# Optimization experiments

Measured on AMD Instinct MI355X. Metric: run time of the kernel, lower is better.

## Reference

```python
import jax, jax.numpy as jnp
import numpy as np

N, C, H, W = 8, 256, 64, 64  # C == dim_inner

def conv1x1(x, w, b):
    # x: [N,C,H,W], w: [O,C], b: [O]  (1x1 conv == per-pixel matmul)
    return jnp.einsum('oc,nchw->nohw', w, x) + b[None, :, None, None]

def setup_inputs() -> dict:
    key = jax.random.key(0)
    ks = jax.random.split(key, 10)
    s = 1.0 / np.sqrt(C)
    return {
        'x':       jax.random.normal(ks[0], (N, C, H, W), dtype=jnp.float32),
        'w_theta': jax.random.uniform(ks[1], (C, C), jnp.float32, -s, s),
        'b_theta': jax.random.uniform(ks[2], (C,),   jnp.float32, -s, s),
        'w_phi':   jax.random.uniform(ks[3], (C, C), jnp.float32, -s, s),
        'b_phi':   jax.random.uniform(ks[4], (C,),   jnp.float32, -s, s),
        'w_g':     jax.random.uniform(ks[5], (C, C), jnp.float32, -s, s),
        'b_g':     jax.random.uniform(ks[6], (C,),   jnp.float32, -s, s),
        'w_out':   jax.random.uniform(ks[7], (C, C), jnp.float32, -s, s),
        'b_out':   jax.random.uniform(ks[8], (C,),   jnp.float32, -s, s),
        'gamma':   jnp.ones((C,), jnp.float32),
        'beta':    jnp.zeros((C,), jnp.float32),
        'w_gate':  jnp.asarray(0.5, jnp.float32),
    }

def reference(x, w_theta, b_theta, w_phi, b_phi, w_g, b_g, w_out, b_out, gamma, beta, w_gate):
    norm_eps = 1e-5
    x_identity = x
    theta = conv1x1(x, w_theta, b_theta).reshape(N, C, H * W)
    phi   = conv1x1(x, w_phi,   b_phi  ).reshape(N, C, H * W)
    g     = conv1x1(x, w_g,     b_g    ).reshape(N, C, H * W)
    # [N, HW, HW] attention scores
    theta_phi = jnp.einsum('nch,ncp->nhp', theta, phi) * (C ** -0.5)
    theta_phi = jax.nn.softmax(theta_phi, axis=2)
    theta_phi_g = jnp.einsum('nhg,ncg->nch', theta_phi, g).reshape(N, C, H, W)
    p = conv1x1(theta_phi_g, w_out, b_out)
    # BatchNorm2d in training mode: batch stats over (N,H,W), biased var
    mean = p.mean(axis=(0, 2, 3))
    var = p.var(axis=(0, 2, 3))
    p = (p - mean[None, :, None, None]) * jax.lax.rsqrt(var + norm_eps)[None, :, None, None]
    p = p * gamma[None, :, None, None] + beta[None, :, None, None]
    z = (1.0 - w_gate) * x_identity + w_gate * p
    return z
```

## Files before the change

kernel.cpp:

```cpp
#include <hip/hip_runtime.h>

#define N_ 8
#define C_ 256
#define HW_ 4096
#define KVBLK 64

typedef __bf16 bf16x8 __attribute__((ext_vector_type(8)));
typedef float f32x4 __attribute__((ext_vector_type(4)));
typedef float f32x16 __attribute__((ext_vector_type(16)));
typedef unsigned short u16x8 __attribute__((ext_vector_type(8)));
typedef unsigned int uint2v __attribute__((ext_vector_type(2)));

#define MFMA(a, b, c)   __builtin_amdgcn_mfma_f32_16x16x32_bf16(a, b, c, 0, 0, 0)
#define MFMA32(a, b, c) __builtin_amdgcn_mfma_f32_32x32x16_bf16(a, b, c, 0, 0, 0)

static __device__ __forceinline__ unsigned short f2bf(float f) {
    union { float f; unsigned int u; } v; v.f = f;
    unsigned int u = v.u;
    return (unsigned short)((u + 0x7FFFu + ((u >> 16) & 1u)) >> 16);
}

static __device__ __forceinline__ bf16x8 pack_bf8(float4 a, float4 b) {
    u16x8 t;
    t[0] = f2bf(a.x); t[1] = f2bf(a.y); t[2] = f2bf(a.z); t[3] = f2bf(a.w);
    t[4] = f2bf(b.x); t[5] = f2bf(b.y); t[6] = f2bf(b.z); t[7] = f2bf(b.w);
    return __builtin_bit_cast(bf16x8, t);
}

static __device__ __forceinline__ unsigned cvt_pk_bf16(float lo, float hi) {
    unsigned r;
    asm("v_cvt_pk_bf16_f32 %0, %1, %2" : "=v"(r) : "v"(lo), "v"(hi));
    return r;
}

static __device__ __forceinline__ void plswap(unsigned& a, unsigned& b) {
#if __has_builtin(__builtin_amdgcn_permlane32_swap)
    uint2v r = __builtin_amdgcn_permlane32_swap(a, b, false, false);
    a = r[0]; b = r[1];
#else
    asm volatile("v_permlane32_swap_b32 %0, %1" : "+v"(a), "+v"(b));
#endif
}

#define GLOAD_LDS16(src, dst)                                                   \
    __builtin_amdgcn_global_load_lds(                                           \
        (const __attribute__((address_space(1))) unsigned int*)(const void*)(src), \
        (__attribute__((address_space(3))) unsigned int*)(void*)(dst), 16, 0, 0)

__global__ __launch_bounds__(256) void qkv_kernel(
    const float* __restrict__ x,
    const float* __restrict__ w_theta, const float* __restrict__ b_theta,
    const float* __restrict__ w_phi,   const float* __restrict__ b_phi,
    const float* __restrict__ w_g,     const float* __restrict__ b_g,
    unsigned short* __restrict__ thetaT, unsigned short* __restrict__ phiT,
    unsigned short* __restrict__ gC)
{
    __shared__ unsigned short xT[64 * 264];
    __shared__ unsigned short tile[64 * 72];
    const int tid = threadIdx.x;
    const int hw0 = blockIdx.x * 64;
    const int n   = blockIdx.y;
    const float* xb = x + (size_t)n * C_ * HW_;
    for (int i = 0; i < 16; ++i) {
        int e   = tid + i * 256;
        int c   = e >> 4;
        int hw4 = (e & 15) << 2;
        float4 v = *reinterpret_cast<const float4*>(xb + (size_t)c * HW_ + hw0 + hw4);
        xT[(hw4 + 0) * 264 + c] = f2bf(v.x);
        xT[(hw4 + 1) * 264 + c] = f2bf(v.y);
        xT[(hw4 + 2) * 264 + c] = f2bf(v.z);
        xT[(hw4 + 3) * 264 + c] = f2bf(v.w);
    }
    __syncthreads();

    const int w = tid >> 6, lane = tid & 63;
    const int g16 = lane >> 4, l16 = lane & 15;

    const float* Wp[3] = { w_theta, w_phi, w_g };
    const float* Bp[3] = { b_theta, b_phi, b_g };

    for (int ot = 0; ot < 4; ++ot) {
        const int oB    = ot * 64;
        const int wrow  = oB + w * 16 + l16;
        const int orow0 = oB + w * 16 + g16 * 4;
        #pragma unroll
        for (int wt = 0; wt < 3; ++wt) {
            const float* W = Wp[wt];
            bf16x8 aw[8];
            #pragma unroll
            for (int kk = 0; kk < 8; ++kk) {
                const float* wp = W + (size_t)wrow * C_ + kk * 32 + g16 * 8;
                float4 f0 = *reinterpret_cast<const float4*>(wp);
                float4 f1 = *reinterpret_cast<const float4*>(wp + 4);
                aw[kk] = pack_bf8(f0, f1);
            }
            f32x4 acc[4];
            #pragma unroll
            for (int cb = 0; cb < 4; ++cb) {
                acc[cb][0] = 0.f; acc[cb][1] = 0.f; acc[cb][2] = 0.f; acc[cb][3] = 0.f;
            }
            #pragma unroll
            for (int kk = 0; kk < 8; ++kk) {
                #pragma unroll
                for (int cb = 0; cb < 4; ++cb) {
                    bf16x8 b = *reinterpret_cast<const bf16x8*>(
                        &xT[(cb * 16 + l16) * 264 + kk * 32 + g16 * 8]);
                    acc[cb] = MFMA(aw[kk], b, acc[cb]);
                }
            }
            const float* bp = Bp[wt];
            float bj0 = bp[orow0], bj1 = bp[orow0 + 1], bj2 = bp[orow0 + 2], bj3 = bp[orow0 + 3];
            if (wt == 2) { bj0 = 0.f; bj1 = 0.f; bj2 = 0.f; bj3 = 0.f; }
            if (wt < 2) {
                const float sc = (wt == 0) ? 0.0625f : 1.0f;
                __syncthreads();
                #pragma unroll
                for (int cb = 0; cb < 4; ++cb) {
                    ushort4 pk;
                    pk.x = f2bf((acc[cb][0] + bj0) * sc);
                    pk.y = f2bf((acc[cb][1] + bj1) * sc);
                    pk.z = f2bf((acc[cb][2] + bj2) * sc);
                    pk.w = f2bf((acc[cb][3] + bj3) * sc);
                    *reinterpret_cast<ushort4*>(&tile[(cb * 16 + l16) * 72 + w * 16 + g16 * 4]) = pk;
                }
                __syncthreads();
                unsigned short* dst = (wt == 0) ? thetaT : phiT;
                #pragma unroll
                for (int i = 0; i < 2; ++i) {
                    int e = tid + i * 256;
                    int row = e >> 3, seg = (e & 7) << 3;
                    *reinterpret_cast<uint4*>(
                        &dst[((size_t)n * HW_ + hw0 + row) * C_ + oB + seg]) =
                        *reinterpret_cast<const uint4*>(&tile[row * 72 + seg]);
                }
            } else {
                #pragma unroll
                for (int cb = 0; cb < 4; ++cb) {
                    int hw = hw0 + cb * 16 + l16;
                    gC[((size_t)n * C_ + orow0 + 0) * HW_ + hw] = f2bf(acc[cb][0]);
                    gC[((size_t)n * C_ + orow0 + 1) * HW_ + hw] = f2bf(acc[cb][1]);
                    gC[((size_t)n * C_ + orow0 + 2) * HW_ + hw] = f2bf(acc[cb][2]);
                    gC[((size_t)n * C_ + orow0 + 3) * HW_ + hw] = f2bf(acc[cb][3]);
                }
            }
        }
    }
}

__global__ __launch_bounds__(256, 1) void attn_kernel(
    const unsigned short* __restrict__ thetaT,
    const unsigned short* __restrict__ phiT,
    const unsigned short* __restrict__ gC,
    unsigned short* __restrict__ tpgT)
{
    __shared__ __align__(16) unsigned short Kbuf[2][64 * 256];
    __shared__ __align__(16) unsigned short Vbuf[2][256 * 64];

    const int tid  = threadIdx.x;
    const int bid  = blockIdx.x;
    const int n    = bid & 7;
    const int qt   = bid >> 3;
    const int w    = tid >> 6, lane = tid & 63;
    const int l31  = lane & 31;
    const int hi   = lane >> 5;
    const int hi8  = hi << 3;

    const unsigned short* Kb = phiT + (size_t)n * HW_ * C_;
    const unsigned short* Vb = gC   + (size_t)n * C_ * HW_;

    bf16x8 qf[16];
    {
        const unsigned short* qp = thetaT + ((size_t)n * HW_ + qt * 128 + w * 32 + l31) * C_;
        #pragma unroll
        for (int kk = 0; kk < 16; ++kk)
            qf[kk] = *reinterpret_cast<const bf16x8*>(qp + kk * 16 + hi8);
    }

    f32x16 oacc[8];
    #pragma unroll
    for (int ncb = 0; ncb < 8; ++ncb)
        #pragma unroll
        for (int r = 0; r < 16; ++r) oacc[ncb][r] = 0.f;
    float m = -1e30f, l = 0.f;

    const int vrow_lane = lane >> 3;
    const int vslot_x   = ((lane & 7) ^ vrow_lane) << 3;

#define STAGE(buf, kv0)                                                          \
    do {                                                                         \
        _Pragma("unroll")                                                        \
        for (int i = 0; i < 8; ++i) {                                            \
            const int rl = w * 16 + i * 2 + hi;                                  \
            const unsigned short* src =                                          \
                Kb + (size_t)((kv0) + rl) * C_ + ((l31 ^ (rl & 31)) << 3);       \
            GLOAD_LDS16(src, &Kbuf[buf][(w * 16 + i * 2) * 256]);                \
        }                                                                        \
        _Pragma("unroll")                                                        \
        for (int i = 0; i < 8; ++i) {                                            \
            const int cr = w * 64 + i * 8 + vrow_lane;                           \
            const unsigned short* src = Vb + (size_t)cr * HW_ + (kv0) + vslot_x; \
            GLOAD_LDS16(src, &Vbuf[buf][(w * 64 + i * 8) * 64]);                 \
        }                                                                        \
    } while (0)

    STAGE(0, 0);
    __syncthreads();

    for (int t = 0; t < 64; ++t) {
        const int cur = t & 1;
        if (t < 63) STAGE(cur ^ 1, (t + 1) * KVBLK);

        f32x16 st[2];
        #pragma unroll
        for (int T = 0; T < 2; ++T) {
            f32x16 sA, sB;
            #pragma unroll
            for (int r = 0; r < 16; ++r) { sA[r] = 0.f; sB[r] = 0.f; }
            const unsigned short* Krow = &Kbuf[cur][(T * 32 + l31) * 256];
            const int swz = l31 << 3;
            #pragma unroll
            for (int kk = 0; kk < 8; ++kk) {
                bf16x8 af = *reinterpret_cast<const bf16x8*>(Krow + (((kk * 16) + hi8) ^ swz));
                sA = MFMA32(af, qf[kk], sA);
            }
            #pragma unroll
            for (int kk = 8; kk < 16; ++kk) {
                bf16x8 af = *reinterpret_cast<const bf16x8*>(Krow + (((kk * 16) + hi8) ^ swz));
                sB = MFMA32(af, qf[kk], sB);
            }
            st[T] = sA + sB;
        }

        float own = st[0][0];
        #pragma unroll
        for (int r = 1; r < 16; ++r) own = fmaxf(own, st[0][r]);
        #pragma unroll
        for (int r = 0; r < 16; ++r) own = fmaxf(own, st[1][r]);
        float pmax = fmaxf(own, __shfl_xor(own, 32));
        if (__any(pmax > m + 8.f)) {
            float mn = fmaxf(m, pmax);
            float f  = __expf(m - mn);
            m = mn; l *= f;
            #pragma unroll
            for (int r = 0; r < 16; ++r) {
                int qr = (r & 3) + 8 * (r >> 2) + (hi8 >> 1);
                float fr = __shfl(f, qr);
                #pragma unroll
                for (int ncb = 0; ncb < 8; ++ncb) oacc[ncb][r] *= fr;
            }
        }
        float lsum = 0.f;
        #pragma unroll
        for (int T = 0; T < 2; ++T)
            #pragma unroll
            for (int r = 0; r < 16; ++r) {
                float e = __expf(st[T][r] - m);
                lsum += e;
                st[T][r] = e;
            }
        l += lsum;

        #pragma unroll
        for (int T = 0; T < 2; ++T) {
            #pragma unroll
            for (int g = 0; g < 2; ++g) {
                unsigned w0 = cvt_pk_bf16(st[T][g * 8 + 0], st[T][g * 8 + 1]);
                unsigned w1 = cvt_pk_bf16(st[T][g * 8 + 2], st[T][g * 8 + 3]);
                unsigned w2 = cvt_pk_bf16(st[T][g * 8 + 4], st[T][g * 8 + 5]);
                unsigned w3 = cvt_pk_bf16(st[T][g * 8 + 6], st[T][g * 8 + 7]);
                plswap(w0, w2);
                plswap(w1, w3);
                uint4 pw; pw.x = w0; pw.y = w1; pw.z = w2; pw.w = w3;
                bf16x8 pf = __builtin_bit_cast(bf16x8, pw);
                const int kk2 = T * 2 + g;
                #pragma unroll
                for (int ncb = 0; ncb < 8; ++ncb) {
                    const int vr = ncb * 32 + l31;
                    bf16x8 vf = *reinterpret_cast<const bf16x8*>(
                        &Vbuf[cur][vr * 64 + (((kk2 * 16) + hi8) ^ ((vr & 7) << 3))]);
                    oacc[ncb] = MFMA32(pf, vf, oacc[ncb]);
                }
            }
        }
        __syncthreads();
    }
#undef STAGE

    float l_tot = l + __shfl_xor(l, 32);
    float inv = 1.0f / l_tot;
    unsigned short* op = tpgT + ((size_t)n * HW_ + qt * 128 + w * 32) * C_;
    #pragma unroll
    for (int r = 0; r < 16; ++r) {
        int qr = (r & 3) + 8 * (r >> 2) + (hi8 >> 1);
        float Lir = __shfl(inv, qr);
        #pragma unroll
        for (int ncb = 0; ncb < 8; ++ncb)
            op[(size_t)qr * C_ + ncb * 32 + l31] = f2bf(oacc[ncb][r] * Lir);
    }
}

__global__ __launch_bounds__(256) void outconv_kernel(
    const unsigned short* __restrict__ tpgT,
    const float* __restrict__ w_out, const float* __restrict__ b_out,
    float* __restrict__ p, float* __restrict__ bnsum, float* __restrict__ bnsumsq)
{
    __shared__ unsigned short Bl[64 * 264];
    const int tid = threadIdx.x;
    const int hw0 = blockIdx.x * 64;
    const int n   = blockIdx.y;
    const unsigned short* Tb = tpgT + (size_t)n * HW_ * C_;
    for (int i = 0; i < 8; ++i) {
        int e = tid + i * 256;
        int r = e >> 5, c8 = (e & 31) << 3;
        *reinterpret_cast<uint4*>(&Bl[r * 264 + c8]) =
            *reinterpret_cast<const uint4*>(Tb + ((size_t)hw0 + r) * C_ + c8);
    }
    __syncthreads();
    const int w = tid >> 6, lane = tid & 63, g16 = lane >> 4, l16 = lane & 15;

    for (int ot = 0; ot < 4; ++ot) {
        const int oB   = ot * 64;
        const int wrow = oB + w * 16 + l16;
        bf16x8 aw[8];
        #pragma unroll
        for (int kk = 0; kk < 8; ++kk) {
            const float* wp = w_out + (size_t)wrow * C_ + kk * 32 + g16 * 8;
            float4 f0 = *reinterpret_cast<const float4*>(wp);
            float4 f1 = *reinterpret_cast<const float4*>(wp + 4);
            aw[kk] = pack_bf8(f0, f1);
        }
        f32x4 acc[4];
        #pragma unroll
        for (int cb = 0; cb < 4; ++cb) { acc[cb][0]=0.f; acc[cb][1]=0.f; acc[cb][2]=0.f; acc[cb][3]=0.f; }
        #pragma unroll
        for (int kk = 0; kk < 8; ++kk) {
            #pragma unroll
            for (int cb = 0; cb < 4; ++cb) {
                bf16x8 b = *reinterpret_cast<const bf16x8*>(
                    &Bl[(cb * 16 + l16) * 264 + kk * 32 + g16 * 8]);
                acc[cb] = MFMA(aw[kk], b, acc[cb]);
            }
        }
        const int orow0 = oB + w * 16 + g16 * 4;
        float bj[4] = { b_out[orow0], b_out[orow0 + 1], b_out[orow0 + 2], b_out[orow0 + 3] };
        float s1[4] = {0.f,0.f,0.f,0.f}, s2[4] = {0.f,0.f,0.f,0.f};
        #pragma unroll
        for (int cb = 0; cb < 4; ++cb) {
            #pragma unroll
            for (int j = 0; j < 4; ++j) {
                float pv = acc[cb][j] + bj[j];
                p[((size_t)n * C_ + orow0 + j) * HW_ + hw0 + cb * 16 + l16] = pv;
                s1[j] += pv;
                s2[j] += pv * pv;
            }
        }
        #pragma unroll
        for (int j = 0; j < 4; ++j) {
            float a1 = s1[j], a2 = s2[j];
            a1 += __shfl_xor(a1, 1); a2 += __shfl_xor(a2, 1);
            a1 += __shfl_xor(a1, 2); a2 += __shfl_xor(a2, 2);
            a1 += __shfl_xor(a1, 4); a2 += __shfl_xor(a2, 4);
            a1 += __shfl_xor(a1, 8); a2 += __shfl_xor(a2, 8);
            if (l16 == 0) {
                atomicAdd(&bnsum[orow0 + j], a1);
                atomicAdd(&bnsumsq[orow0 + j], a2);
            }
        }
    }
}

__global__ void bnfin_kernel(const float* __restrict__ bnsum,
                             const float* __restrict__ bnsumsq,
                             const float* __restrict__ gamma,
                             const float* __restrict__ beta,
                             float* __restrict__ bnscale, float* __restrict__ bnshift)
{
    int c = threadIdx.x;
    const float cnt = (float)(N_ * HW_);
    float mean = bnsum[c] / cnt;
    float var  = bnsumsq[c] / cnt - mean * mean;
    float inv  = rsqrtf(var + 1e-5f);
    float sc   = gamma[c] * inv;
    bnscale[c] = sc;
    bnshift[c] = beta[c] - mean * sc;
}

__global__ __launch_bounds__(256) void final_kernel(
    const float* __restrict__ x, const float* __restrict__ p,
    const float* __restrict__ bnscale, const float* __restrict__ bnshift,
    const float* __restrict__ wgate, float* __restrict__ out)
{
    const float wg = *wgate;
    const float og = 1.0f - wg;
    const int total = N_ * C_ * HW_ / 4;
    for (int e = blockIdx.x * 256 + threadIdx.x; e < total; e += gridDim.x * 256) {
        int c = (e >> 10) & 255;
        float sc = bnscale[c], sh = bnshift[c];
        float4 xv = reinterpret_cast<const float4*>(x)[e];
        float4 pv = reinterpret_cast<const float4*>(p)[e];
        float4 z;
        z.x = og * xv.x + wg * (pv.x * sc + sh);
        z.y = og * xv.y + wg * (pv.y * sc + sh);
        z.z = og * xv.z + wg * (pv.z * sc + sh);
        z.w = og * xv.w + wg * (pv.w * sc + sh);
        reinterpret_cast<float4*>(out)[e] = z;
    }
}

extern "C" void kernel_launch(void* const* d_in, const int* in_sizes, int n_in,
                              void* d_out, int out_size, void* d_ws, size_t ws_size,
                              hipStream_t stream)
{
    (void)in_sizes; (void)n_in; (void)out_size; (void)ws_size;
    const float* x       = (const float*)d_in[0];
    const float* w_theta = (const float*)d_in[1];
    const float* b_theta = (const float*)d_in[2];
    const float* w_phi   = (const float*)d_in[3];
    const float* b_phi   = (const float*)d_in[4];
    const float* w_g     = (const float*)d_in[5];
    const float* b_g     = (const float*)d_in[6];
    const float* w_out   = (const float*)d_in[7];
    const float* b_out   = (const float*)d_in[8];
    const float* gamma   = (const float*)d_in[9];
    const float* beta    = (const float*)d_in[10];
    const float* wgate   = (const float*)d_in[11];
    float* out = (float*)d_out;

    char* ws = (char*)d_ws;
    unsigned short* thetaT = (unsigned short*)(ws + 0);
    unsigned short* phiT   = (unsigned short*)(ws + 16777216);
    unsigned short* gC     = (unsigned short*)(ws + 33554432);
    unsigned short* tpgT   = (unsigned short*)(ws + 50331648);
    float* p       = (float*)(ws + 0);
    float* bnsum   = (float*)(ws + 67108864);
    float* bnsumsq = (float*)(ws + 67108864 + 1024);
    float* bnscale = (float*)(ws + 67108864 + 2048);
    float* bnshift = (float*)(ws + 67108864 + 3072);

    hipMemsetAsync(bnsum, 0, 2048, stream);

    qkv_kernel<<<dim3(64, 8), 256, 0, stream>>>(
        x, w_theta, b_theta, w_phi, b_phi, w_g, b_g, thetaT, phiT, gC);
    attn_kernel<<<dim3(256), 256, 0, stream>>>(thetaT, phiT, gC, tpgT);
    outconv_kernel<<<dim3(64, 8), 256, 0, stream>>>(tpgT, w_out, b_out, p, bnsum, bnsumsq);
    bnfin_kernel<<<1, 256, 0, stream>>>(bnsum, bnsumsq, gamma, beta, bnscale, bnshift);
    final_kernel<<<dim3(2048), 256, 0, stream>>>(x, p, bnscale, bnshift, wgate, out);
}
```

Measured before the change: 480.7 us.

## Split attention over two KV halves with a merge kernel

Adds a split-KV flash attention path. Each block handles a 128-query tile over half of the keys, using 32-wide KV stages and two blocks per CU, which doubles the grid to 512 blocks to improve occupancy and load balance on 256 CUs. Partial outputs in bf16 and the (m, l) statistics are written to workspace, and a separate merge kernel combines them by log-sum-exp rescaling. This costs extra global traffic, one more launch and an additional bf16 rounding of the partials. The original kernel stays as a fallback when the workspace is too small.

Result: slower. 492.5 us (+2.4%).

```diff
diff --git a/kernel.cpp b/kernel.cpp
--- a/kernel.cpp
+++ b/kernel.cpp
@@ -3,7 +3,6 @@
 #define N_ 8
 #define C_ 256
 #define HW_ 4096
-#define KVBLK 64
 
 typedef __bf16 bf16x8 __attribute__((ext_vector_type(8)));
 typedef float f32x4 __attribute__((ext_vector_type(4)));
@@ -18,6 +17,10 @@
     union { float f; unsigned int u; } v; v.f = f;
     unsigned int u = v.u;
     return (unsigned short)((u + 0x7FFFu + ((u >> 16) & 1u)) >> 16);
+}
+
+static __device__ __forceinline__ float bfu2f(unsigned s) {
+    union { unsigned u; float f; } v; v.u = s << 16; return v.f;
 }
 
 static __device__ __forceinline__ bf16x8 pack_bf8(float4 a, float4 b) {
@@ -147,7 +150,189 @@
     }
 }
 
-__global__ __launch_bounds__(256, 1) void attn_kernel(
+__global__ __launch_bounds__(256, 2) void attn_split_kernel(
+    const unsigned short* __restrict__ thetaT,
+    const unsigned short* __restrict__ phiT,
+    const unsigned short* __restrict__ gC,
+    unsigned short* __restrict__ Opart,
+    float2* __restrict__ ml)
+{
+    __shared__ __align__(16) unsigned short Kbuf[2][32 * 256];
+    __shared__ __align__(16) unsigned short Vbuf[2][256 * 32];
+
+    const int tid  = threadIdx.x;
+    const int bid  = blockIdx.x;
+    const int n    = bid & 7;
+    const int enc  = bid >> 3;
+    const int qt   = enc >> 1;
+    const int kvh  = enc & 1;
+    const int w    = tid >> 6, lane = tid & 63;
+    const int l31  = lane & 31;
+    const int hi   = lane >> 5;
+    const int hi8  = hi << 3;
+    const int kvbase = kvh * 2048;
+
+    const unsigned short* Kb = phiT + (size_t)n * HW_ * C_;
+    const unsigned short* Vb = gC   + (size_t)n * C_ * HW_;
+
+    bf16x8 qf[16];
+    {
+        const unsigned short* qp = thetaT + ((size_t)n * HW_ + qt * 128 + w * 32 + l31) * C_;
+        #pragma unroll
+        for (int kk = 0; kk < 16; ++kk)
+            qf[kk] = *reinterpret_cast<const bf16x8*>(qp + kk * 16 + hi8);
+    }
+
+    f32x16 oacc[8];
+    #pragma unroll
+    for (int ncb = 0; ncb < 8; ++ncb)
+        #pragma unroll
+        for (int r = 0; r < 16; ++r) oacc[ncb][r] = 0.f;
+    float m = -1e30f, l = 0.f;
+
+    const int vrow_lane = lane >> 2;
+    const int vslot     = lane & 3;
+
+#define STAGE(buf, kv0)                                                          \
+    do {                                                                         \
+        _Pragma("unroll")                                                        \
+        for (int i = 0; i < 4; ++i) {                                            \
+            const int rl = w * 8 + i * 2 + hi;                                   \
+            const unsigned short* src =                                          \
+                Kb + (size_t)((kv0) + rl) * C_ + ((l31 ^ rl) << 3);              \
+            GLOAD_LDS16(src, &Kbuf[buf][(w * 8 + i * 2) * 256]);                 \
+        }                                                                        \
+        _Pragma("unroll")                                                        \
+        for (int i = 0; i < 4; ++i) {                                            \
+            const int cr = w * 64 + i * 16 + vrow_lane;                          \
+            const unsigned short* src =                                          \
+                Vb + (size_t)cr * HW_ + (kv0) + ((vslot ^ ((cr >> 1) & 3)) << 3);\
+            GLOAD_LDS16(src, &Vbuf[buf][(w * 64 + i * 16) * 32]);                \
+        }                                                                        \
+    } while (0)
+
+    STAGE(0, kvbase);
+    __syncthreads();
+
+    for (int t = 0; t < 64; ++t) {
+        const int cur = t & 1;
+        if (t < 63) STAGE(cur ^ 1, kvbase + (t + 1) * 32);
+
+        f32x16 sA, sB;
+        #pragma unroll
+        for (int r = 0; r < 16; ++r) { sA[r] = 0.f; sB[r] = 0.f; }
+        const unsigned short* Krow = &Kbuf[cur][l31 * 256];
+        const int swz = l31 << 3;
+        #pragma unroll
+        for (int kk = 0; kk < 8; ++kk) {
+            bf16x8 af = *reinterpret_cast<const bf16x8*>(Krow + (((kk * 16) + hi8) ^ swz));
+            sA = MFMA32(af, qf[kk], sA);
+        }
+        #pragma unroll
+        for (int kk = 8; kk < 16; ++kk) {
+            bf16x8 af = *reinterpret_cast<const bf16x8*>(Krow + (((kk * 16) + hi8) ^ swz));
+            sB = MFMA32(af, qf[kk], sB);
+        }
+        f32x16 s = sA + sB;
+
+        float own = s[0];
+        #pragma unroll
+        for (int r = 1; r < 16; ++r) own = fmaxf(own, s[r]);
+        float pmax = fmaxf(own, __shfl_xor(own, 32));
+        if (__any(pmax > m + 8.f)) {
+            float mn = fmaxf(m, pmax);
+            float f  = __expf(m - mn);
+            m = mn; l *= f;
+            #pragma unroll
+            for (int r = 0; r < 16; ++r) {
+                int qr = (r & 3) + 8 * (r >> 2) + (hi8 >> 1);
+                float fr = __shfl(f, qr);
+                #pragma unroll
+                for (int ncb = 0; ncb < 8; ++ncb) oacc[ncb][r] *= fr;
+            }
+        }
+        float lsum = 0.f;
+        #pragma unroll
+        for (int r = 0; r < 16; ++r) {
+            float ex = __expf(s[r] - m);
+            lsum += ex;
+            s[r] = ex;
+        }
+        l += lsum;
+
+        #pragma unroll
+        for (int g = 0; g < 2; ++g) {
+            unsigned w0 = cvt_pk_bf16(s[g * 8 + 0], s[g * 8 + 1]);
+            unsigned w1 = cvt_pk_bf16(s[g * 8 + 2], s[g * 8 + 3]);
+            unsigned w2 = cvt_pk_bf16(s[g * 8 + 4], s[g * 8 + 5]);
+            unsigned w3 = cvt_pk_bf16(s[g * 8 + 6], s[g * 8 + 7]);
+            plswap(w0, w2);
+            plswap(w1, w3);
+            uint4 pw; pw.x = w0; pw.y = w1; pw.z = w2; pw.w = w3;
+            bf16x8 pf = __builtin_bit_cast(bf16x8, pw);
+            #pragma unroll
+            for (int ncb = 0; ncb < 8; ++ncb) {
+                const int vr = ncb * 32 + l31;
+                bf16x8 vf = *reinterpret_cast<const bf16x8*>(
+                    &Vbuf[cur][vr * 32 + (((g * 16) + hi8) ^ (((vr >> 1) & 3) << 3))]);
+                oacc[ncb] = MFMA32(pf, vf, oacc[ncb]);
+            }
+        }
+        __syncthreads();
+    }
+#undef STAGE
+
+    float l_tot = l + __shfl_xor(l, 32);
+    #pragma unroll
+    for (int r = 0; r < 16; ++r) {
+        int qr = (r & 3) + 8 * (r >> 2) + (hi8 >> 1);
+        #pragma unroll
+        for (int ncb = 0; ncb < 8; ++ncb)
+            Opart[((size_t)bid * 128 + w * 32 + qr) * 256 + ncb * 32 + l31] =
+                f2bf(oacc[ncb][r]);
+    }
+    if (lane < 32)
+        ml[(size_t)bid * 128 + w * 32 + l31] = make_float2(m, l_tot);
+}
+
+__global__ __launch_bounds__(256) void merge_kernel(
+    const unsigned short* __restrict__ Opart,
+    const float2* __restrict__ ml,
+    unsigned short* __restrict__ tpgT)
+{
+    const int b   = blockIdx.x;
+    const int n   = b & 7, qt = b >> 3;
+    const int tid = threadIdx.x;
+    const int r8  = tid >> 5;
+    const int c8  = (tid & 31) * 8;
+    const int b0  = ((qt * 2 + 0) << 3) | n;
+    const int b1  = ((qt * 2 + 1) << 3) | n;
+    for (int it = 0; it < 16; ++it) {
+        const int q = it * 8 + r8;
+        float2 a1 = ml[(size_t)b0 * 128 + q];
+        float2 a2 = ml[(size_t)b1 * 128 + q];
+        float M  = fmaxf(a1.x, a2.x);
+        float f1 = __expf(a1.x - M);
+        float f2 = __expf(a2.x - M);
+        float Li = 1.0f / (a1.y * f1 + a2.y * f2);
+        uint4 o1 = *reinterpret_cast<const uint4*>(&Opart[((size_t)b0 * 128 + q) * 256 + c8]);
+        uint4 o2 = *reinterpret_cast<const uint4*>(&Opart[((size_t)b1 * 128 + q) * 256 + c8]);
+        uint4 ov;
+        const unsigned* p1 = reinterpret_cast<const unsigned*>(&o1);
+        const unsigned* p2 = reinterpret_cast<const unsigned*>(&o2);
+        unsigned* po = reinterpret_cast<unsigned*>(&ov);
+        #pragma unroll
+        for (int k = 0; k < 4; ++k) {
+            float vlo = (bfu2f(p1[k] & 0xffffu) * f1 + bfu2f(p2[k] & 0xffffu) * f2) * Li;
+            float vhi = (bfu2f(p1[k] >> 16)     * f1 + bfu2f(p2[k] >> 16)     * f2) * Li;
+            po[k] = cvt_pk_bf16(vlo, vhi);
+        }
+        *reinterpret_cast<uint4*>(
+            &tpgT[((size_t)n * HW_ + qt * 128 + q) * 256 + c8]) = ov;
+    }
+}
+
+__global__ __launch_bounds__(256, 1) void attn_full_kernel(
     const unsigned short* __restrict__ thetaT,
     const unsigned short* __restrict__ phiT,
     const unsigned short* __restrict__ gC,
@@ -208,7 +393,7 @@
 
     for (int t = 0; t < 64; ++t) {
         const int cur = t & 1;
-        if (t < 63) STAGE(cur ^ 1, (t + 1) * KVBLK);
+        if (t < 63) STAGE(cur ^ 1, (t + 1) * 64);
 
         f32x16 st[2];
         #pragma unroll
@@ -254,9 +439,9 @@
         for (int T = 0; T < 2; ++T)
             #pragma unroll
             for (int r = 0; r < 16; ++r) {
-                float e = __expf(st[T][r] - m);
-                lsum += e;
-                st[T][r] = e;
+                float ex = __expf(st[T][r] - m);
+                lsum += ex;
+                st[T][r] = ex;
             }
         l += lsum;
 
@@ -411,7 +596,7 @@
                               void* d_out, int out_size, void* d_ws, size_t ws_size,
                               hipStream_t stream)
 {
-    (void)in_sizes; (void)n_in; (void)out_size; (void)ws_size;
+    (void)in_sizes; (void)n_in; (void)out_size;
     const float* x       = (const float*)d_in[0];
     const float* w_theta = (const float*)d_in[1];
     const float* b_theta = (const float*)d_in[2];
@@ -430,19 +615,41 @@
     unsigned short* thetaT = (unsigned short*)(ws + 0);
     unsigned short* phiT   = (unsigned short*)(ws + 16777216);
     unsigned short* gC     = (unsigned short*)(ws + 33554432);
-    unsigned short* tpgT   = (unsigned short*)(ws + 50331648);
-    float* p       = (float*)(ws + 0);
-    float* bnsum   = (float*)(ws + 67108864);
-    float* bnsumsq = (float*)(ws + 67108864 + 1024);
-    float* bnscale = (float*)(ws + 67108864 + 2048);
-    float* bnshift = (float*)(ws + 67108864 + 3072);
-
-    hipMemsetAsync(bnsum, 0, 2048, stream);
-
-    qkv_kernel<<<dim3(64, 8), 256, 0, stream>>>(
-        x, w_theta, b_theta, w_phi, b_phi, w_g, b_g, thetaT, phiT, gC);
-    attn_kernel<<<dim3(256), 256, 0, stream>>>(thetaT, phiT, gC, tpgT);
-    outconv_kernel<<<dim3(64, 8), 256, 0, stream>>>(tpgT, w_out, b_out, p, bnsum, bnsumsq);
-    bnfin_kernel<<<1, 256, 0, stream>>>(bnsum, bnsumsq, gamma, beta, bnscale, bnshift);
-    final_kernel<<<dim3(2048), 256, 0, stream>>>(x, p, bnscale, bnshift, wgate, out);
-}
+    float* p = (float*)(ws + 0);
+
+    const size_t NEED_SPLIT = 84414464ull;
+    const bool use_split = ws_size >= NEED_SPLIT;
+
+    if (use_split) {
+        unsigned short* tpgT  = (unsigned short*)(ws + 33554432);
+        unsigned short* Opart = (unsigned short*)(ws + 50331648);
+        float2*         mlp   = (float2*)(ws + 83886080);
+        float* bnsum   = (float*)(ws + 84410368);
+        float* bnsumsq = (float*)(ws + 84410368 + 1024);
+        float* bnscale = (float*)(ws + 84410368 + 2048);
+        float* bnshift = (float*)(ws + 84410368 + 3072);
+
+        hipMemsetAsync(bnsum, 0, 2048, stream);
+        qkv_kernel<<<dim3(64, 8), 256, 0, stream>>>(
+            x, w_theta, b_theta, w_phi, b_phi, w_g, b_g, thetaT, phiT, gC);
+        attn_split_kernel<<<dim3(512), 256, 0, stream>>>(thetaT, phiT, gC, Opart, mlp);
+        merge_kernel<<<dim3(256), 256, 0, stream>>>(Opart, mlp, tpgT);
+        outconv_kernel<<<dim3(64, 8), 256, 0, stream>>>(tpgT, w_out, b_out, p, bnsum, bnsumsq);
+        bnfin_kernel<<<1, 256, 0, stream>>>(bnsum, bnsumsq, gamma, beta, bnscale, bnshift);
+        final_kernel<<<dim3(2048), 256, 0, stream>>>(x, p, bnscale, bnshift, wgate, out);
+    } else {
+        unsigned short* tpgT = (unsigned short*)(ws + 50331648);
+        float* bnsum   = (float*)(ws + 67108864);
+        float* bnsumsq = (float*)(ws + 67108864 + 1024);
+        float* bnscale = (float*)(ws + 67108864 + 2048);
+        float* bnshift = (float*)(ws + 67108864 + 3072);
+
+        hipMemsetAsync(bnsum, 0, 2048, stream);
+        qkv_kernel<<<dim3(64, 8), 256, 0, stream>>>(
+            x, w_theta, b_theta, w_phi, b_phi, w_g, b_g, thetaT, phiT, gC);
+        attn_full_kernel<<<dim3(256), 256, 0, stream>>>(thetaT, phiT, gC, tpgT);
+        outconv_kernel<<<dim3(64, 8), 256, 0, stream>>>(tpgT, w_out, b_out, p, bnsum, bnsumsq);
+        bnfin_kernel<<<1, 256, 0, stream>>>(bnsum, bnsumsq, gamma, beta, bnscale, bnshift);
+        final_kernel<<<dim3(2048), 256, 0, stream>>>(x, p, bnscale, bnshift, wgate, out);
+    }
+}
```
